# Kernel tuning notes

Measured on AMD Instinct MI355X. Metric: run time of the kernel, lower is better.

## Reference

```python
import jax, jax.numpy as jnp
import numpy as np

D = 256      # in_out_dimension
HID = 128    # hidden_dimension
N = 8192     # total nodes
S = 256      # number of graphs/segments


def setup_inputs() -> dict:
    key = jax.random.key(0)
    ks = jax.random.split(key, 20)
    lin = lambda k, o, i: jax.random.normal(k, (o, i), jnp.float32) * 0.05
    vec = lambda k, o: jax.random.normal(k, (o,), jnp.float32) * 0.05
    H = jax.random.normal(ks[0], (N, D), jnp.float32)
    batch = jnp.sort(jax.random.randint(ks[1], (N,), 0, S)).astype(jnp.int64)
    return {
        "H": H, "batch": batch,
        "phi_w1": lin(ks[2], D, D), "phi_b1": vec(ks[3], D),
        "phi_w2": lin(ks[4], D, D), "phi_b2": vec(ks[5], D),
        "att_w": lin(ks[6], D, D), "att_b": vec(ks[7], D),
        "rho_w1": lin(ks[8], D, D), "rho_b1": vec(ks[9], D),
        "rho_w2": lin(ks[10], D, D), "rho_b2": vec(ks[11], D),
        "g_w1": lin(ks[12], HID, D), "g_b1": vec(ks[13], HID),
        "g_w2": lin(ks[14], HID, HID), "g_b2": vec(ks[15], HID),
        "g_w3": lin(ks[16], 1, HID), "g_b3": vec(ks[17], 1),
    }


def _lrelu(x):
    return jax.nn.leaky_relu(x, negative_slope=0.01)


def reference(H, batch, phi_w1, phi_b1, phi_w2, phi_b2, att_w, att_b,
              rho_w1, rho_b1, rho_w2, rho_b2,
              g_w1, g_b1, g_w2, g_b2, g_w3, g_b3):
    # phi MLP
    Hf = _lrelu(_lrelu(H @ phi_w1.T + phi_b1) @ phi_w2.T + phi_b2)  # [N, D]
    att = Hf @ att_w.T + att_b                                      # [N, D]
    dot = att @ att.T                                               # [N, N]
    mask = (batch[:, None] == batch[None, :]).astype(Hf.dtype)      # block-diagonal
    # faithful to torch: max over (dot * mask), i.e. includes masked zeros
    max_values = jnp.max(dot * mask, axis=1, keepdims=True)         # [N, 1]
    mdp = (dot - max_values) * mask
    e = jnp.exp(mdp)
    aw = (e / jnp.sum(e * mask, axis=1, keepdims=True)) * mask      # [N, N]
    H_mixed = aw @ Hf                                               # [N, D]
    H_mixed = _lrelu(_lrelu(H_mixed @ rho_w1.T + rho_b1) @ rho_w2.T + rho_b2)
    h_gate = _lrelu(_lrelu(H_mixed @ g_w1.T + g_b1) @ g_w2.T + g_b2) @ g_w3.T + g_b3  # [N, 1]
    # scatter_softmax over segments
    seg_max = jax.ops.segment_max(h_gate, batch, num_segments=S)    # [S, 1]
    ex = jnp.exp(h_gate - seg_max[batch])
    den = jax.ops.segment_sum(ex, batch, num_segments=S)
    scores = ex / den[batch]                                        # [N, 1]
    h_pool = jax.ops.segment_sum(H_mixed * scores, batch, num_segments=S)  # [S, D]
    return (h_pool, scores)
```

## Files before the change

kernel.cpp:

```cpp
#include <hip/hip_runtime.h>
#include <math.h>

#define N_NODES 8192
#define D 256
#define HID 128
#define S_SEG 256
#define MAXC 64
#define PST 65

typedef __attribute__((ext_vector_type(8))) short short8;
typedef __attribute__((ext_vector_type(4))) float f32x4;
typedef unsigned short u16;
typedef unsigned int u32;

__device__ __forceinline__ u16 f2bf(float f) {
  u32 u = __float_as_uint(f);
  u32 r = (u + 0x7fffu + ((u >> 16) & 1u)) >> 16;
  return (u16)r;
}
__device__ __forceinline__ float bf2f(u16 b) {
  return __uint_as_float(((u32)b) << 16);
}
__device__ __forceinline__ int4 pack8(float4 x, float4 y) {
  int4 v;
  v.x = (int)(((u32)f2bf(x.y) << 16) | f2bf(x.x));
  v.y = (int)(((u32)f2bf(x.w) << 16) | f2bf(x.z));
  v.z = (int)(((u32)f2bf(y.y) << 16) | f2bf(y.x));
  v.w = (int)(((u32)f2bf(y.w) << 16) | f2bf(y.z));
  return v;
}

struct CvtJobs {
  const float* src[7];
  u16* dst[7];
  int n4[7];
};
__global__ __launch_bounds__(256) void prep(const int* __restrict__ batch,
                                            int* __restrict__ sstart,
                                            int* __restrict__ scount, CvtJobs jb) {
  if (blockIdx.x == 0) {
    __shared__ int cntS[S_SEG];
    __shared__ int startS[S_SEG];
    const int t = threadIdx.x;
    cntS[t] = 0;
    startS[t] = 0;
    __syncthreads();
    const int base = t * 32;
    int pb = (base == 0) ? -1 : batch[base - 1];
    for (int i = 0; i < 32; ++i) {
      int b = batch[base + i];
      atomicAdd(&cntS[b], 1);
      if (b != pb) startS[b] = base + i;
      pb = b;
    }
    __syncthreads();
    scount[t] = cntS[t];
    sstart[t] = startS[t];
  } else {
    const int bid = blockIdx.x - 1;
    const int job = bid >> 3, chunk = bid & 7;
    const float* s = jb.src[job];
    u16* d = jb.dst[job];
    const int n4 = jb.n4[job];
    for (int i = chunk * 256 + threadIdx.x; i < n4; i += 2048) {
      float4 v = ((const float4*)s)[i];
      ushort4 o;
      o.x = f2bf(v.x); o.y = f2bf(v.y); o.z = f2bf(v.z); o.w = f2bf(v.w);
      ((ushort4*)d)[i] = o;
    }
  }
}

template <int KST>
__device__ __forceinline__ void loadW(short8* w, const u16* __restrict__ Wg,
                                      int col, int K, int lane) {
  const u16* base = Wg + (size_t)col * K + ((lane >> 4) * 8);
#pragma unroll
  for (int kk = 0; kk < KST; ++kk) w[kk] = *(const short8*)(base + kk * 32);
}

template <int KST, int ACT, int ISTR, int OSTR, int MODE, int MG>
__device__ __forceinline__ void mlp_phase(
    const u16* ldsIn, u16* ldsOut, u16* ldsOut2, const short8* wreg,
    const float* __restrict__ bias, int cg, int rows, int lane, int wave) {
  const int nrt = (rows + 31) >> 5;
  const int col = cg * 16 + (lane & 15);
  const float b = bias[col];
  int rt0, rt1;
  if constexpr (MG == 16) {
    rt0 = 0; rt1 = nrt;
  } else {
    rt0 = wave >> 3;
    rt1 = (rt0 < nrt) ? rt0 + 1 : rt0;
  }
  for (int rt = rt0; rt < rt1; ++rt) {
    short8 af[2][KST];
#pragma unroll
    for (int m = 0; m < 2; ++m)
#pragma unroll
      for (int kk = 0; kk < KST; ++kk) {
        const int r = rt * 32 + m * 16 + (lane & 15);
        const int sl = kk * 4 + (lane >> 4);
        af[m][kk] = *(const short8*)((const char*)ldsIn + r * ISTR +
                                     ((sl ^ (r & 7)) * 16));
      }
    f32x4 acc0 = {0.f, 0.f, 0.f, 0.f}, acc1 = {0.f, 0.f, 0.f, 0.f};
#pragma unroll
    for (int kk = 0; kk < KST; ++kk) {
      acc0 = __builtin_amdgcn_mfma_f32_16x16x32_bf16(af[0][kk], wreg[kk], acc0, 0, 0, 0);
      acc1 = __builtin_amdgcn_mfma_f32_16x16x32_bf16(af[1][kk], wreg[kk], acc1, 0, 0, 0);
    }
    const int rb = (lane >> 4) * 4;
#pragma unroll
    for (int m = 0; m < 2; ++m) {
      f32x4 a = m ? acc1 : acc0;
#pragma unroll
      for (int r4 = 0; r4 < 4; ++r4) {
        const int row = rt * 32 + m * 16 + rb + r4;
        if (row < rows) {
          float v = a[r4] + b;
          if (ACT) v = (v >= 0.f) ? v : 0.01f * v;
          if constexpr (MODE == 3) {
            const int byo =
                row * OSTR + (((col >> 3) ^ (row & 7)) * 16) + (col & 7) * 2;
            u16 hi = f2bf(v);
            *(u16*)((char*)ldsOut + byo) = hi;
            *(u16*)((char*)ldsOut2 + byo) = f2bf(v - bf2f(hi));
          } else {
            *(u16*)((char*)ldsOut + row * OSTR +
                    (((col >> 3) ^ (row & 7)) * 16) + (col & 7) * 2) = f2bf(v);
          }
        }
      }
    }
  }
}

template <int KST, int ACT, int ISTR, int OSTR, int MODE>
__device__ __forceinline__ void mlp16(
    const u16* ldsIn, u16* ldsOut, u16* ldsOut2, const u16* __restrict__ Wg,
    const float* __restrict__ bias, u16* __restrict__ gOut,
    u16* __restrict__ gOut2, int M, int K, int rows, int lane, int wave) {
  const int MG = M >> 4;
  const int npairs = ((rows + 31) >> 5) * MG;
  for (int p = wave; p < npairs; p += 16) {
    const int rt = p / MG, cg = p - rt * MG;
    short8 af[2][KST];
#pragma unroll
    for (int m = 0; m < 2; ++m)
#pragma unroll
      for (int kk = 0; kk < KST; ++kk) {
        const int r = rt * 32 + m * 16 + (lane & 15);
        const int sl = kk * 4 + (lane >> 4);
        af[m][kk] = *(const short8*)((const char*)ldsIn + r * ISTR +
                                     ((sl ^ (r & 7)) * 16));
      }
    const int col = cg * 16 + (lane & 15);
    short8 bfr[KST];
#pragma unroll
    for (int kk = 0; kk < KST; ++kk)
      bfr[kk] = *(const short8*)&Wg[(size_t)col * K + kk * 32 + (lane >> 4) * 8];
    f32x4 acc0 = {0.f, 0.f, 0.f, 0.f}, acc1 = {0.f, 0.f, 0.f, 0.f};
#pragma unroll
    for (int kk = 0; kk < KST; ++kk) {
      acc0 = __builtin_amdgcn_mfma_f32_16x16x32_bf16(af[0][kk], bfr[kk], acc0, 0, 0, 0);
      acc1 = __builtin_amdgcn_mfma_f32_16x16x32_bf16(af[1][kk], bfr[kk], acc1, 0, 0, 0);
    }
    const float b = bias[col];
    const int rb = (lane >> 4) * 4;
#pragma unroll
    for (int m = 0; m < 2; ++m) {
      f32x4 a = m ? acc1 : acc0;
#pragma unroll
      for (int r4 = 0; r4 < 4; ++r4) {
        const int row = rt * 32 + m * 16 + rb + r4;
        if (row < rows) {
          float v = a[r4] + b;
          if (ACT) v = (v >= 0.f) ? v : 0.01f * v;
          if constexpr (MODE == 2) {
            u16 hi = f2bf(v);
            gOut[(size_t)row * M + col] = hi;
            gOut2[(size_t)row * M + col] = f2bf(v - bf2f(hi));
          } else if constexpr (MODE == 3) {
            const int byo =
                row * OSTR + (((col >> 3) ^ (row & 7)) * 16) + (col & 7) * 2;
            u16 hi = f2bf(v);
            *(u16*)((char*)ldsOut + byo) = hi;
            *(u16*)((char*)ldsOut2 + byo) = f2bf(v - bf2f(hi));
          } else {
            u16 hv = f2bf(v);
            *(u16*)((char*)ldsOut + row * OSTR + (((col >> 3) ^ (row & 7)) * 16) +
                    (col & 7) * 2) = hv;
            if constexpr (MODE == 1) gOut[(size_t)row * M + col] = hv;
          }
        }
      }
    }
  }
}

__global__ __launch_bounds__(1024) void seg_all(
    const float* __restrict__ H, const u16* __restrict__ pw1,
    const float* __restrict__ pb1, const u16* __restrict__ pw2,
    const float* __restrict__ pb2, const u16* __restrict__ aw,
    const float* __restrict__ ab, const u16* __restrict__ rw1,
    const float* __restrict__ rb1, const u16* __restrict__ rw2,
    const float* __restrict__ rb2, const u16* __restrict__ gw1,
    const float* __restrict__ gb1, const u16* __restrict__ gw2,
    const float* __restrict__ gb2, const float* __restrict__ gw3,
    const float* __restrict__ gb3, const int* __restrict__ sstart,
    const int* __restrict__ scount, float* __restrict__ hpool,
    float* __restrict__ scores, u16* __restrict__ Hfg, u16* __restrict__ aHg,
    u16* __restrict__ aLg, u16* __restrict__ Hmg, u16* __restrict__ Hm2g,
    float* __restrict__ hgg) {
  __shared__ __align__(16) u16 bufX[MAXC * 256];
  __shared__ __align__(16) u16 bufY[MAXC * 256];
  __shared__ __align__(16) u16 attH[MAXC * 256];
  __shared__ __align__(16) u16 attL[MAXC * 256];
  __shared__ float hgs[MAXC];
  __shared__ float red[1024];
  __shared__ float part[1024];
  const int s = blockIdx.x, t = threadIdx.x;
  const int cnt = scount[s];
  const int r0 = sstart[s];
  const int wave = t >> 6, lane = t & 63;

  if (cnt == 0) {
    if (t < 256) hpool[(size_t)s * D + t] = 0.f;
    return;
  }

  if (cnt <= MAXC) {
    short8 wreg[8];
    const int cg16 = (wave + s) & 15;
    const int cg8 = ((wave & 7) + s) & 7;
    const int col16 = cg16 * 16 + (lane & 15);
    const int col8 = cg8 * 16 + (lane & 15);

    loadW<8>(wreg, pw1, col16, D, lane);
    {
      const int r = t >> 4, p16 = t & 15;
      if (r < cnt) {
        const float4* src = (const float4*)&H[(size_t)(r0 + r) * D + p16 * 16];
#pragma unroll
        for (int i = 0; i < 2; ++i) {
          int4 v = pack8(src[2 * i], src[2 * i + 1]);
          const int sl = p16 * 2 + i;
          *(int4*)((char*)bufX + r * 512 + ((sl ^ (r & 7)) * 16)) = v;
        }
      }
    }
    __syncthreads();
    mlp_phase<8, 1, 512, 512, 0, 16>(bufX, bufY, nullptr, wreg, pb1, cg16, cnt, lane, wave);
    loadW<8>(wreg, pw2, col16, D, lane);
    __syncthreads();
    mlp_phase<8, 1, 512, 512, 0, 16>(bufY, bufX, nullptr, wreg, pb2, cg16, cnt, lane, wave);
    loadW<8>(wreg, aw, col16, D, lane);
    __syncthreads();
    mlp_phase<8, 0, 512, 512, 3, 16>(bufX, attH, attL, wreg, ab, cg16, cnt, lane, wave);
    __syncthreads();
    float* P = (float*)bufY;
    const int cp = (cnt + 15) & ~15;
    const int nt = cp >> 4;
    const int lrow = lane & 15;
    for (int tt = wave; tt < nt * nt; tt += 16) {
      const int ti = tt / nt, tj = tt - ti * nt;
      const int ra = ti * 16 + lrow, rb2 = tj * 16 + lrow;
      f32x4 acc = {0.f, 0.f, 0.f, 0.f};
#pragma unroll
      for (int k0 = 0; k0 < D; k0 += 32) {
        const int sg = (k0 >> 3) + (lane >> 4);
        short8 ah = *(const short8*)((const char*)attH + ra * 512 + ((sg ^ (ra & 7)) * 16));
        short8 av = *(const short8*)((const char*)attL + ra * 512 + ((sg ^ (ra & 7)) * 16));
        short8 bh = *(const short8*)((const char*)attH + rb2 * 512 + ((sg ^ (rb2 & 7)) * 16));
        short8 bv = *(const short8*)((const char*)attL + rb2 * 512 + ((sg ^ (rb2 & 7)) * 16));
        acc = __builtin_amdgcn_mfma_f32_16x16x32_bf16(ah, bh, acc, 0, 0, 0);
        acc = __builtin_amdgcn_mfma_f32_16x16x32_bf16(ah, bv, acc, 0, 0, 0);
        acc = __builtin_amdgcn_mfma_f32_16x16x32_bf16(av, bh, acc, 0, 0, 0);
      }
      const int i0 = ti * 16 + (lane >> 4) * 4, j = tj * 16 + lrow;
#pragma unroll
      for (int r = 0; r < 4; ++r) P[(i0 + r) * PST + j] = acc[r];
    }
    __syncthreads();
    loadW<8>(wreg, rw1, col16, D, lane);
    for (int i = wave; i < cnt; i += 16) {
      const float v = (lane < cnt) ? P[i * PST + lane] : -INFINITY;
      float m = v;
#pragma unroll
      for (int o = 32; o > 0; o >>= 1) m = fmaxf(m, __shfl_xor(m, o));
      float e = (lane < cnt) ? __expf(v - m) : 0.f;
      float sum = e;
#pragma unroll
      for (int o = 32; o > 0; o >>= 1) sum += __shfl_xor(sum, o);
      e *= 1.f / sum;
      float a0 = 0.f, a1 = 0.f, a2 = 0.f, a3 = 0.f;
      for (int j = 0; j < cnt; ++j) {
        const float wj = __shfl(e, j);
        const ushort4 hv = *(const ushort4*)((const char*)bufX + j * 512 +
                             (((lane >> 1) ^ (j & 7)) * 16) + (lane & 1) * 8);
        a0 += wj * bf2f(hv.x);
        a1 += wj * bf2f(hv.y);
        a2 += wj * bf2f(hv.z);
        a3 += wj * bf2f(hv.w);
      }
      ushort4 o;
      o.x = f2bf(a0); o.y = f2bf(a1); o.z = f2bf(a2); o.w = f2bf(a3);
      *(ushort4*)((char*)attH + i * 512 + (((lane >> 1) ^ (i & 7)) * 16) +
                  (lane & 1) * 8) = o;
    }
    __syncthreads();
    mlp_phase<8, 1, 512, 512, 0, 16>(attH, attL, nullptr, wreg, rb1, cg16, cnt, lane, wave);
    loadW<8>(wreg, rw2, col16, D, lane);
    __syncthreads();
    mlp_phase<8, 1, 512, 512, 0, 16>(attL, bufX, nullptr, wreg, rb2, cg16, cnt, lane, wave);
    loadW<8>(wreg, gw1, col8, D, lane);
    __syncthreads();
    mlp_phase<8, 1, 512, 256, 0, 8>(bufX, bufY, nullptr, wreg, gb1, cg8, cnt, lane, wave);
    loadW<4>(wreg, gw2, col8, HID, lane);
    __syncthreads();
    mlp_phase<4, 1, 256, 256, 0, 8>(bufY, attH, nullptr, wreg, gb2, cg8, cnt, lane, wave);
    __syncthreads();
    {
      const int i = t >> 4, p16 = t & 15;
      if (i < cnt) {
        short8 hv = *(const short8*)((const char*)attH + i * 256 + ((p16 ^ (i & 7)) * 16));
        float sacc = 0.f;
#pragma unroll
        for (int q = 0; q < 8; ++q) sacc += bf2f((u16)hv[q]) * gw3[p16 * 8 + q];
        sacc += __shfl_xor(sacc, 1);
        sacc += __shfl_xor(sacc, 2);
        sacc += __shfl_xor(sacc, 4);
        sacc += __shfl_xor(sacc, 8);
        if (p16 == 0) hgs[i] = sacc + gb3[0];
      }
    }
    __syncthreads();
    if (t < 64) {
      float v = (t < cnt) ? hgs[t] : -INFINITY;
      float m = v;
#pragma unroll
      for (int o = 32; o > 0; o >>= 1) m = fmaxf(m, __shfl_xor(m, o));
      float e = (t < cnt) ? __expf(v - m) : 0.f;
      float sum = e;
#pragma unroll
      for (int o = 32; o > 0; o >>= 1) sum += __shfl_xor(sum, o);
      if (t < cnt) {
        const float sc = e / sum;
        hgs[t] = sc;
        scores[r0 + t] = sc;
      }
    }
    __syncthreads();
    {
      const int h = t >> 8, d = t & 255;
      float acc = 0.f;
      for (int i = h; i < cnt; i += 4)
        acc += hgs[i] * bf2f(*(const u16*)((const char*)bufX + i * 512 +
                              (((d >> 3) ^ (i & 7)) * 16) + (d & 7) * 2));
      part[t] = acc;
    }
    __syncthreads();
    if (t < 256)
      hpool[(size_t)s * D + t] =
          part[t] + part[t + 256] + part[t + 512] + part[t + 768];
  } else {
    for (int c0 = 0; c0 < cnt; c0 += 64) {
      const int rows = (cnt - c0) > 64 ? 64 : (cnt - c0);
      {
        const int r = t >> 4, p16 = t & 15;
        if (r < rows) {
          const float4* src = (const float4*)&H[(size_t)(r0 + c0 + r) * D + p16 * 16];
#pragma unroll
          for (int i = 0; i < 2; ++i) {
            int4 v = pack8(src[2 * i], src[2 * i + 1]);
            const int sl = p16 * 2 + i;
            *(int4*)((char*)bufX + r * 512 + ((sl ^ (r & 7)) * 16)) = v;
          }
        }
      }
      __syncthreads();
      mlp16<8, 1, 512, 512, 0>(bufX, bufY, nullptr, pw1, pb1, nullptr, nullptr, D, D, rows, lane, wave);
      __syncthreads();
      mlp16<8, 1, 512, 512, 1>(bufY, bufX, nullptr, pw2, pb2, Hfg + (size_t)(r0 + c0) * D, nullptr, D, D, rows, lane, wave);
      __syncthreads();
      mlp16<8, 0, 512, 512, 2>(bufX, nullptr, nullptr, aw, ab, aHg + (size_t)(r0 + c0) * D, aLg + (size_t)(r0 + c0) * D, D, D, rows, lane, wave);
      __syncthreads();
    }
    float* Pf = (float*)bufY;
    for (int i = 0; i < cnt; ++i) {
      const u16* ai = aHg + (size_t)(r0 + i) * D;
      const u16* li = aLg + (size_t)(r0 + i) * D;
      for (int j = t; j < cnt; j += 1024) {
        const u16* aj = aHg + (size_t)(r0 + j) * D;
        const u16* lj = aLg + (size_t)(r0 + j) * D;
        float acc = 0.f;
        for (int k = 0; k < D; ++k)
          acc += (bf2f(ai[k]) + bf2f(li[k])) * (bf2f(aj[k]) + bf2f(lj[k]));
        Pf[j] = acc;
      }
      __syncthreads();
      float pm = -INFINITY;
      for (int j = t; j < cnt; j += 1024) pm = fmaxf(pm, Pf[j]);
      red[t] = pm;
      __syncthreads();
      for (int o = 512; o > 0; o >>= 1) {
        if (t < o) red[t] = fmaxf(red[t], red[t + o]);
        __syncthreads();
      }
      const float m = red[0];
      __syncthreads();
      float ps = 0.f;
      for (int j = t; j < cnt; j += 1024) {
        const float e = __expf(Pf[j] - m);
        Pf[j] = e;
        ps += e;
      }
      red[t] = ps;
      __syncthreads();
      for (int o = 512; o > 0; o >>= 1) {
        if (t < o) red[t] += red[t + o];
        __syncthreads();
      }
      const float inv = 1.f / red[0];
      if (t < D) {
        float acc = 0.f;
        for (int j = 0; j < cnt; ++j)
          acc += Pf[j] * bf2f(Hfg[(size_t)(r0 + j) * D + t]);
        Hmg[(size_t)(r0 + i) * D + t] = f2bf(acc * inv);
      }
      __syncthreads();
    }
    for (int c0 = 0; c0 < cnt; c0 += 64) {
      const int rows = (cnt - c0) > 64 ? 64 : (cnt - c0);
      {
        const int r = t >> 4, p16 = t & 15;
        if (r < rows) {
          const int4* src = (const int4*)&Hmg[(size_t)(r0 + c0 + r) * D + p16 * 16];
#pragma unroll
          for (int i = 0; i < 2; ++i) {
            const int sl = p16 * 2 + i;
            *(int4*)((char*)bufX + r * 512 + ((sl ^ (r & 7)) * 16)) = src[i];
          }
        }
      }
      __syncthreads();
      mlp16<8, 1, 512, 512, 0>(bufX, bufY, nullptr, rw1, rb1, nullptr, nullptr, D, D, rows, lane, wave);
      __syncthreads();
      mlp16<8, 1, 512, 512, 1>(bufY, bufX, nullptr, rw2, rb2, Hm2g + (size_t)(r0 + c0) * D, nullptr, D, D, rows, lane, wave);
      __syncthreads();
      mlp16<8, 1, 512, 256, 0>(bufX, bufY, nullptr, gw1, gb1, nullptr, nullptr, HID, D, rows, lane, wave);
      __syncthreads();
      mlp16<4, 1, 256, 256, 0>(bufY, attH, nullptr, gw2, gb2, nullptr, nullptr, HID, HID, rows, lane, wave);
      __syncthreads();
      {
        const int i = t >> 4, p16 = t & 15;
        if (i < rows) {
          short8 hv = *(const short8*)((const char*)attH + i * 256 + ((p16 ^ (i & 7)) * 16));
          float sacc = 0.f;
#pragma unroll
          for (int q = 0; q < 8; ++q) sacc += bf2f((u16)hv[q]) * gw3[p16 * 8 + q];
          sacc += __shfl_xor(sacc, 1);
          sacc += __shfl_xor(sacc, 2);
          sacc += __shfl_xor(sacc, 4);
          sacc += __shfl_xor(sacc, 8);
          if (p16 == 0) hgg[r0 + c0 + i] = sacc + gb3[0];
        }
      }
      __syncthreads();
    }
    float pm = -INFINITY;
    for (int i = t; i < cnt; i += 1024) pm = fmaxf(pm, hgg[r0 + i]);
    red[t] = pm;
    __syncthreads();
    for (int o = 512; o > 0; o >>= 1) {
      if (t < o) red[t] = fmaxf(red[t], red[t + o]);
      __syncthreads();
    }
    const float m = red[0];
    __syncthreads();
    float ps = 0.f;
    for (int i = t; i < cnt; i += 1024) ps += __expf(hgg[r0 + i] - m);
    red[t] = ps;
    __syncthreads();
    for (int o = 512; o > 0; o >>= 1) {
      if (t < o) red[t] += red[t + o];
      __syncthreads();
    }
    const float inv = 1.f / red[0];
    for (int i = t; i < cnt; i += 1024)
      scores[r0 + i] = __expf(hgg[r0 + i] - m) * inv;
    const int h = t >> 8, d = t & 255;
    float acc = 0.f;
    for (int i = h; i < cnt; i += 4)
      acc += __expf(hgg[r0 + i] - m) * inv * bf2f(Hm2g[(size_t)(r0 + i) * D + d]);
    part[t] = acc;
    __syncthreads();
    if (t < 256)
      hpool[(size_t)s * D + t] =
          part[t] + part[t + 256] + part[t + 512] + part[t + 768];
  }
}

extern "C" void kernel_launch(void* const* d_in, const int* in_sizes, int n_in,
                              void* d_out, int out_size, void* d_ws, size_t ws_size,
                              hipStream_t stream) {
  const float* H      = (const float*)d_in[0];
  const int*   batch  = (const int*)d_in[1];
  const float* phi_w1 = (const float*)d_in[2];
  const float* phi_b1 = (const float*)d_in[3];
  const float* phi_w2 = (const float*)d_in[4];
  const float* phi_b2 = (const float*)d_in[5];
  const float* att_w  = (const float*)d_in[6];
  const float* att_b  = (const float*)d_in[7];
  const float* rho_w1 = (const float*)d_in[8];
  const float* rho_b1 = (const float*)d_in[9];
  const float* rho_w2 = (const float*)d_in[10];
  const float* rho_b2 = (const float*)d_in[11];
  const float* g_w1   = (const float*)d_in[12];
  const float* g_b1   = (const float*)d_in[13];
  const float* g_w2   = (const float*)d_in[14];
  const float* g_b2   = (const float*)d_in[15];
  const float* g_w3   = (const float*)d_in[16];
  const float* g_b3   = (const float*)d_in[17];

  float* out_hpool  = (float*)d_out;
  float* out_scores = (float*)d_out + (size_t)S_SEG * D;

  char* w = (char*)d_ws;
  const size_t MB = 1u << 20;
  u16*   wb     = (u16*)(w);
  u16*   Hfg    = (u16*)(w + 1 * MB);
  u16*   aHg    = (u16*)(w + 5 * MB);
  u16*   aLg    = (u16*)(w + 9 * MB);
  u16*   Hmg    = (u16*)(w + 13 * MB);
  u16*   Hm2g   = (u16*)(w + 17 * MB);
  float* hgg    = (float*)(w + 21 * MB);
  int*   sstart = (int*)(w + 21 * MB + 64 * 1024);
  int*   scount = sstart + S_SEG;

  u16* phi_w1b = wb;
  u16* phi_w2b = wb + 65536;
  u16* att_wb  = wb + 2 * 65536;
  u16* rho_w1b = wb + 3 * 65536;
  u16* rho_w2b = wb + 4 * 65536;
  u16* g_w1b   = wb + 5 * 65536;
  u16* g_w2b   = wb + 5 * 65536 + 32768;

  CvtJobs jb;
  jb.src[0] = phi_w1; jb.dst[0] = phi_w1b; jb.n4[0] = 65536 / 4;
  jb.src[1] = phi_w2; jb.dst[1] = phi_w2b; jb.n4[1] = 65536 / 4;
  jb.src[2] = att_w;  jb.dst[2] = att_wb;  jb.n4[2] = 65536 / 4;
  jb.src[3] = rho_w1; jb.dst[3] = rho_w1b; jb.n4[3] = 65536 / 4;
  jb.src[4] = rho_w2; jb.dst[4] = rho_w2b; jb.n4[4] = 65536 / 4;
  jb.src[5] = g_w1;   jb.dst[5] = g_w1b;   jb.n4[5] = 32768 / 4;
  jb.src[6] = g_w2;   jb.dst[6] = g_w2b;   jb.n4[6] = 16384 / 4;

  prep<<<57, 256, 0, stream>>>(batch, sstart, scount, jb);

  seg_all<<<S_SEG, 1024, 0, stream>>>(
      H, phi_w1b, phi_b1, phi_w2b, phi_b2, att_wb, att_b, rho_w1b, rho_b1,
      rho_w2b, rho_b2, g_w1b, g_b1, g_w2b, g_b2, g_w3, g_b3, sstart, scount,
      out_hpool, out_scores, Hfg, aHg, aLg, Hmg, Hm2g, hgg);
}
```

Measured before the change: 60.55 us.

## Use MFMA for attention-weighted mixing and fuse gate tail into MLP epilogue

Replaces the scalar per-row softmax plus shuffle-based aw@Hf loop with an MFMA path. The Hf output is written transposed into a new LDS buffer, softmax numerators and row sums are computed straight from the QK accumulators, and P is split into hi/lo bf16 for the MFMA product. The exp is applied without max subtraction, so it relies on logits staying small. The final gate layer and its w3 dot product are fused into a custom MFMA epilogue using LDS atomics, and the segment-softmax and pooling stages are merged to drop syncthreads. The trade-offs are extra LDS traffic from the transposed write and zero padding, and possible overflow if logits grow.

Result: faster. 52.57 us (-13.2%).

```diff
diff --git a/kernel.cpp b/kernel.cpp
--- a/kernel.cpp
+++ b/kernel.cpp
@@ -6,7 +6,9 @@
 #define HID 128
 #define S_SEG 256
 #define MAXC 64
-#define PST 65
+#define HFT_STR 144
+#define PB_STR 144
+#define PB_LO 9216
 
 typedef __attribute__((ext_vector_type(8))) short short8;
 typedef __attribute__((ext_vector_type(4))) float f32x4;
@@ -126,6 +128,11 @@
             u16 hi = f2bf(v);
             *(u16*)((char*)ldsOut + byo) = hi;
             *(u16*)((char*)ldsOut2 + byo) = f2bf(v - bf2f(hi));
+          } else if constexpr (MODE == 4) {
+            u16 hv = f2bf(v);
+            *(u16*)((char*)ldsOut + row * OSTR +
+                    (((col >> 3) ^ (row & 7)) * 16) + (col & 7) * 2) = hv;
+            *(u16*)((char*)ldsOut2 + col * HFT_STR + row * 2) = hv;
           } else {
             *(u16*)((char*)ldsOut + row * OSTR +
                     (((col >> 3) ^ (row & 7)) * 16) + (col & 7) * 2) = f2bf(v);
@@ -181,12 +188,6 @@
             u16 hi = f2bf(v);
             gOut[(size_t)row * M + col] = hi;
             gOut2[(size_t)row * M + col] = f2bf(v - bf2f(hi));
-          } else if constexpr (MODE == 3) {
-            const int byo =
-                row * OSTR + (((col >> 3) ^ (row & 7)) * 16) + (col & 7) * 2;
-            u16 hi = f2bf(v);
-            *(u16*)((char*)ldsOut + byo) = hi;
-            *(u16*)((char*)ldsOut2 + byo) = f2bf(v - bf2f(hi));
           } else {
             u16 hv = f2bf(v);
             *(u16*)((char*)ldsOut + row * OSTR + (((col >> 3) ^ (row & 7)) * 16) +
@@ -216,7 +217,8 @@
   __shared__ __align__(16) u16 bufX[MAXC * 256];
   __shared__ __align__(16) u16 bufY[MAXC * 256];
   __shared__ __align__(16) u16 attH[MAXC * 256];
-  __shared__ __align__(16) u16 attL[MAXC * 256];
+  __shared__ __align__(16) u16 Tt[256 * 72];
+  __shared__ float redP[64][4];
   __shared__ float hgs[MAXC];
   __shared__ float red[1024];
   __shared__ float part[1024];
@@ -236,6 +238,7 @@
     const int cg8 = ((wave & 7) + s) & 7;
     const int col16 = cg16 * 16 + (lane & 15);
     const int col8 = cg8 * 16 + (lane & 15);
+    const int lrow = lane & 15;
 
     loadW<8>(wreg, pw1, col16, D, lane);
     {
@@ -254,111 +257,182 @@
     mlp_phase<8, 1, 512, 512, 0, 16>(bufX, bufY, nullptr, wreg, pb1, cg16, cnt, lane, wave);
     loadW<8>(wreg, pw2, col16, D, lane);
     __syncthreads();
-    mlp_phase<8, 1, 512, 512, 0, 16>(bufY, bufX, nullptr, wreg, pb2, cg16, cnt, lane, wave);
+    mlp_phase<8, 1, 512, 512, 4, 16>(bufY, bufX, (u16*)Tt, wreg, pb2, cg16, cnt, lane, wave);
     loadW<8>(wreg, aw, col16, D, lane);
     __syncthreads();
-    mlp_phase<8, 0, 512, 512, 3, 16>(bufX, attH, attL, wreg, ab, cg16, cnt, lane, wave);
-    __syncthreads();
-    float* P = (float*)bufY;
+    mlp_phase<8, 0, 512, 512, 3, 16>(bufX, attH, bufY, wreg, ab, cg16, cnt, lane, wave);
+    __syncthreads();
     const int cp = (cnt + 15) & ~15;
     const int nt = cp >> 4;
-    const int lrow = lane & 15;
-    for (int tt = wave; tt < nt * nt; tt += 16) {
-      const int ti = tt / nt, tj = tt - ti * nt;
+    f32x4 ev = {0.f, 0.f, 0.f, 0.f};
+    const int ttile = wave;
+    const bool qact = ttile < nt * nt;
+    int ti = 0, tj = 0;
+    if (qact) {
+      ti = ttile / nt; tj = ttile - ti * nt;
       const int ra = ti * 16 + lrow, rb2 = tj * 16 + lrow;
       f32x4 acc = {0.f, 0.f, 0.f, 0.f};
 #pragma unroll
       for (int k0 = 0; k0 < D; k0 += 32) {
         const int sg = (k0 >> 3) + (lane >> 4);
         short8 ah = *(const short8*)((const char*)attH + ra * 512 + ((sg ^ (ra & 7)) * 16));
-        short8 av = *(const short8*)((const char*)attL + ra * 512 + ((sg ^ (ra & 7)) * 16));
+        short8 av = *(const short8*)((const char*)bufY + ra * 512 + ((sg ^ (ra & 7)) * 16));
         short8 bh = *(const short8*)((const char*)attH + rb2 * 512 + ((sg ^ (rb2 & 7)) * 16));
-        short8 bv = *(const short8*)((const char*)attL + rb2 * 512 + ((sg ^ (rb2 & 7)) * 16));
+        short8 bv = *(const short8*)((const char*)bufY + rb2 * 512 + ((sg ^ (rb2 & 7)) * 16));
         acc = __builtin_amdgcn_mfma_f32_16x16x32_bf16(ah, bh, acc, 0, 0, 0);
         acc = __builtin_amdgcn_mfma_f32_16x16x32_bf16(ah, bv, acc, 0, 0, 0);
         acc = __builtin_amdgcn_mfma_f32_16x16x32_bf16(av, bh, acc, 0, 0, 0);
       }
-      const int i0 = ti * 16 + (lane >> 4) * 4, j = tj * 16 + lrow;
-#pragma unroll
-      for (int r = 0; r < 4; ++r) P[(i0 + r) * PST + j] = acc[r];
-    }
-    __syncthreads();
+      const int j = tj * 16 + lrow;
+      const bool jok = j < cnt;
+#pragma unroll
+      for (int r = 0; r < 4; ++r) ev[r] = jok ? __expf(acc[r]) : 0.f;
+      float p0 = ev[0], p1 = ev[1], p2 = ev[2], p3 = ev[3];
+#pragma unroll
+      for (int o = 1; o <= 8; o <<= 1) {
+        p0 += __shfl_xor(p0, o); p1 += __shfl_xor(p1, o);
+        p2 += __shfl_xor(p2, o); p3 += __shfl_xor(p3, o);
+      }
+      if ((lane & 15) == 0) {
+        const int rbase = ti * 16 + (lane >> 4) * 4;
+        redP[rbase + 0][tj] = p0;
+        redP[rbase + 1][tj] = p1;
+        redP[rbase + 2][tj] = p2;
+        redP[rbase + 3][tj] = p3;
+      }
+    }
+    __syncthreads();
+    const int cpk = (cp <= 32) ? 32 : 64;
+    if (qact) {
+      const int j = tj * 16 + lrow;
+      const int rbase = ti * 16 + (lane >> 4) * 4;
+#pragma unroll
+      for (int r = 0; r < 4; ++r) {
+        float rs = 0.f;
+        for (int q = 0; q < nt; ++q) rs += redP[rbase + r][q];
+        const float pv = ev[r] / rs;
+        const u16 hi = f2bf(pv);
+        const u16 lo = f2bf(pv - bf2f(hi));
+        *(u16*)((char*)bufY + (rbase + r) * PB_STR + j * 2) = hi;
+        *(u16*)((char*)bufY + PB_LO + (rbase + r) * PB_STR + j * 2) = lo;
+      }
+    }
+    if (cpk > cp) {
+      const int w2 = cpk - cp;
+      for (int idx = t; idx < cp * w2; idx += 1024) {
+        const int rr = idx / w2, cc = cp + idx - (idx / w2) * w2;
+        *(u16*)((char*)bufY + rr * PB_STR + cc * 2) = 0;
+        *(u16*)((char*)bufY + PB_LO + rr * PB_STR + cc * 2) = 0;
+      }
+    }
+    if (cpk > cnt) {
+      const int w3 = cpk - cnt;
+      for (int idx = t; idx < 256 * w3; idx += 1024) {
+        const int dd = idx / w3, cc = cnt + idx - (idx / w3) * w3;
+        *(u16*)((char*)Tt + dd * HFT_STR + cc * 2) = 0;
+      }
+    }
+    __syncthreads();
+    {
+      const int kst = cpk >> 5;
+      for (int tt = wave; tt < nt * 16; tt += 16) {
+        const int rt = tt >> 4, cg = tt & 15;
+        const int arow = rt * 16 + lrow;
+        const int dcol = cg * 16 + lrow;
+        const int koct = (lane >> 4) * 8;
+        f32x4 acc = {0.f, 0.f, 0.f, 0.f};
+        for (int ks = 0; ks < kst; ++ks) {
+          const int kb = ks * 32 + koct;
+          short8 ph = *(const short8*)((const char*)bufY + arow * PB_STR + kb * 2);
+          short8 pl = *(const short8*)((const char*)bufY + PB_LO + arow * PB_STR + kb * 2);
+          short8 hb = *(const short8*)((const char*)Tt + dcol * HFT_STR + kb * 2);
+          acc = __builtin_amdgcn_mfma_f32_16x16x32_bf16(ph, hb, acc, 0, 0, 0);
+          acc = __builtin_amdgcn_mfma_f32_16x16x32_bf16(pl, hb, acc, 0, 0, 0);
+        }
+        const int rb = (lane >> 4) * 4;
+#pragma unroll
+        for (int r = 0; r < 4; ++r) {
+          const int row = rt * 16 + rb + r;
+          const int col = cg * 16 + lrow;
+          *(u16*)((char*)bufX + row * 512 + (((col >> 3) ^ (row & 7)) * 16) +
+                  (col & 7) * 2) = f2bf(acc[r]);
+        }
+      }
+    }
     loadW<8>(wreg, rw1, col16, D, lane);
-    for (int i = wave; i < cnt; i += 16) {
-      const float v = (lane < cnt) ? P[i * PST + lane] : -INFINITY;
-      float m = v;
+    __syncthreads();
+    mlp_phase<8, 1, 512, 512, 0, 16>(bufX, attH, nullptr, wreg, rb1, cg16, cnt, lane, wave);
+    loadW<8>(wreg, rw2, col16, D, lane);
+    __syncthreads();
+    mlp_phase<8, 1, 512, 512, 0, 16>(attH, (u16*)Tt, nullptr, wreg, rb2, cg16, cnt, lane, wave);
+    loadW<8>(wreg, gw1, col8, D, lane);
+    __syncthreads();
+    if (t < 64) hgs[t] = 0.f;
+    mlp_phase<8, 1, 512, 256, 0, 8>((u16*)Tt, bufX, nullptr, wreg, gb1, cg8, cnt, lane, wave);
+    loadW<4>(wreg, gw2, col8, HID, lane);
+    __syncthreads();
+    {
+      const int nrt = (cnt + 31) >> 5;
+      const int rt = wave >> 3;
+      if (rt < nrt) {
+        short8 af2[2][4];
+#pragma unroll
+        for (int m = 0; m < 2; ++m)
+#pragma unroll
+          for (int kk = 0; kk < 4; ++kk) {
+            const int r = rt * 32 + m * 16 + (lane & 15);
+            const int sl = kk * 4 + (lane >> 4);
+            af2[m][kk] = *(const short8*)((const char*)bufX + r * 256 +
+                                          ((sl ^ (r & 7)) * 16));
+          }
+        f32x4 acc0 = {0.f, 0.f, 0.f, 0.f}, acc1 = {0.f, 0.f, 0.f, 0.f};
+#pragma unroll
+        for (int kk = 0; kk < 4; ++kk) {
+          acc0 = __builtin_amdgcn_mfma_f32_16x16x32_bf16(af2[0][kk], wreg[kk], acc0, 0, 0, 0);
+          acc1 = __builtin_amdgcn_mfma_f32_16x16x32_bf16(af2[1][kk], wreg[kk], acc1, 0, 0, 0);
+        }
+        const float b = gb2[col8];
+        const float w3c = gw3[col8];
+        const int rb = (lane >> 4) * 4;
+#pragma unroll
+        for (int m = 0; m < 2; ++m) {
+          f32x4 a = m ? acc1 : acc0;
+#pragma unroll
+          for (int r4 = 0; r4 < 4; ++r4) {
+            const int row = rt * 32 + m * 16 + rb + r4;
+            float v = a[r4] + b;
+            v = (v >= 0.f) ? v : 0.01f * v;
+            float pp = v * w3c;
+            pp += __shfl_xor(pp, 1);
+            pp += __shfl_xor(pp, 2);
+            pp += __shfl_xor(pp, 4);
+            pp += __shfl_xor(pp, 8);
+            if ((lane & 15) == 0 && row < cnt) atomicAdd(&hgs[row], pp);
+          }
+        }
+      }
+    }
+    __syncthreads();
+    {
+      const float hgv = (lane < cnt) ? hgs[lane] : -INFINITY;
+      float m = hgv;
 #pragma unroll
       for (int o = 32; o > 0; o >>= 1) m = fmaxf(m, __shfl_xor(m, o));
-      float e = (lane < cnt) ? __expf(v - m) : 0.f;
+      float e = (lane < cnt) ? __expf(hgv - m) : 0.f;
       float sum = e;
 #pragma unroll
       for (int o = 32; o > 0; o >>= 1) sum += __shfl_xor(sum, o);
-      e *= 1.f / sum;
-      float a0 = 0.f, a1 = 0.f, a2 = 0.f, a3 = 0.f;
-      for (int j = 0; j < cnt; ++j) {
-        const float wj = __shfl(e, j);
-        const ushort4 hv = *(const ushort4*)((const char*)bufX + j * 512 +
-                             (((lane >> 1) ^ (j & 7)) * 16) + (lane & 1) * 8);
-        a0 += wj * bf2f(hv.x);
-        a1 += wj * bf2f(hv.y);
-        a2 += wj * bf2f(hv.z);
-        a3 += wj * bf2f(hv.w);
-      }
-      ushort4 o;
-      o.x = f2bf(a0); o.y = f2bf(a1); o.z = f2bf(a2); o.w = f2bf(a3);
-      *(ushort4*)((char*)attH + i * 512 + (((lane >> 1) ^ (i & 7)) * 16) +
-                  (lane & 1) * 8) = o;
-    }
-    __syncthreads();
-    mlp_phase<8, 1, 512, 512, 0, 16>(attH, attL, nullptr, wreg, rb1, cg16, cnt, lane, wave);
-    loadW<8>(wreg, rw2, col16, D, lane);
-    __syncthreads();
-    mlp_phase<8, 1, 512, 512, 0, 16>(attL, bufX, nullptr, wreg, rb2, cg16, cnt, lane, wave);
-    loadW<8>(wreg, gw1, col8, D, lane);
-    __syncthreads();
-    mlp_phase<8, 1, 512, 256, 0, 8>(bufX, bufY, nullptr, wreg, gb1, cg8, cnt, lane, wave);
-    loadW<4>(wreg, gw2, col8, HID, lane);
-    __syncthreads();
-    mlp_phase<4, 1, 256, 256, 0, 8>(bufY, attH, nullptr, wreg, gb2, cg8, cnt, lane, wave);
-    __syncthreads();
-    {
-      const int i = t >> 4, p16 = t & 15;
-      if (i < cnt) {
-        short8 hv = *(const short8*)((const char*)attH + i * 256 + ((p16 ^ (i & 7)) * 16));
-        float sacc = 0.f;
-#pragma unroll
-        for (int q = 0; q < 8; ++q) sacc += bf2f((u16)hv[q]) * gw3[p16 * 8 + q];
-        sacc += __shfl_xor(sacc, 1);
-        sacc += __shfl_xor(sacc, 2);
-        sacc += __shfl_xor(sacc, 4);
-        sacc += __shfl_xor(sacc, 8);
-        if (p16 == 0) hgs[i] = sacc + gb3[0];
-      }
-    }
-    __syncthreads();
-    if (t < 64) {
-      float v = (t < cnt) ? hgs[t] : -INFINITY;
-      float m = v;
-#pragma unroll
-      for (int o = 32; o > 0; o >>= 1) m = fmaxf(m, __shfl_xor(m, o));
-      float e = (t < cnt) ? __expf(v - m) : 0.f;
-      float sum = e;
-#pragma unroll
-      for (int o = 32; o > 0; o >>= 1) sum += __shfl_xor(sum, o);
-      if (t < cnt) {
-        const float sc = e / sum;
-        hgs[t] = sc;
-        scores[r0 + t] = sc;
-      }
-    }
-    __syncthreads();
-    {
-      const int h = t >> 8, d = t & 255;
+      const float sc = e / sum;
+      if (wave == 0 && lane < cnt) scores[r0 + lane] = sc;
+      const int d = (wave & 3) * 64 + lane;
+      const int g = wave >> 2;
       float acc = 0.f;
-      for (int i = h; i < cnt; i += 4)
-        acc += hgs[i] * bf2f(*(const u16*)((const char*)bufX + i * 512 +
-                              (((d >> 3) ^ (i & 7)) * 16) + (d & 7) * 2));
-      part[t] = acc;
+      for (int i = g; i < cnt; i += 4) {
+        const float si = __shfl(sc, i);
+        acc += si * bf2f(*(const u16*)((const char*)Tt + i * 512 +
+                          (((d >> 3) ^ (i & 7)) * 16) + (d & 7) * 2));
+      }
+      part[g * 256 + d] = acc;
     }
     __syncthreads();
     if (t < 256)
```
